# Kernel tuning notes

Hardware: AMD Instinct MI355X
Metric: run time of the kernel (lower is better)

## Reference

```python
import jax, jax.numpy as jnp
import numpy as np

D_SVG, N_TYPE, N_PAR = 256, 10, 12          # deep-svg latent, animation types, animation params
PADDING_VALUE = -1.0
W_SVG, W_TYPE, W_PAR = 10.0, 0.1, 1.0       # weight_deep_svg, weight_type, weight_parameters

# ANIMATION_PARAMETER_INDICES as a dense boolean lookup: type t -> which params it uses
_pm = np.zeros((N_TYPE, N_PAR), dtype=bool)
for _t in range(N_TYPE):
    for _k in (_t % N_PAR, (_t + 1) % N_PAR, (_t + 2) % N_PAR):
        _pm[_t, _k] = True
PARAM_MASK = jnp.asarray(_pm)


def setup_inputs() -> dict:
    B, S = 256, 512
    F = D_SVG + N_TYPE + N_PAR
    key = jax.random.key(0)
    k1, k2, k3, k4, k5 = jax.random.split(key, 5)
    x = jax.random.normal(k1, (B, S, F), dtype=jnp.float32)
    cls = jax.random.randint(k2, (B, S), 0, N_TYPE)
    t_type = jax.nn.one_hot(cls, N_TYPE, dtype=jnp.float32)
    t_svg = jax.random.normal(k3, (B, S, D_SVG), dtype=jnp.float32)
    t_par = jax.random.normal(k4, (B, S, N_PAR), dtype=jnp.float32)
    target = jnp.concatenate([t_svg, t_type, t_par], axis=-1)
    # suffix-contiguous padding (matches the `break` semantics of the torch loop)
    lengths = jax.random.randint(k5, (B,), S // 2, S + 1)
    mask = jnp.arange(S)[None, :] >= lengths[:, None]            # True = padded
    target = jnp.where(mask[..., None], PADDING_VALUE, target)
    return {"input": x, "target": target, "target_padding_mask": mask}


def reference(input, target, target_padding_mask):
    # input[expanded_mask] = -100
    x = jnp.where(target_padding_mask[..., None], -100.0, input)
    in_svg, in_type, in_par = jnp.split(x, [D_SVG, D_SVG + N_TYPE], axis=-1)
    tg_svg, tg_type, tg_par = jnp.split(target, [D_SVG, D_SVG + N_TYPE], axis=-1)

    valid = tg_type[..., 0] != PADDING_VALUE                      # [B,S] non-padded rows
    t_idx = jnp.argmax(tg_type, axis=-1)                          # [B,S] animation type

    # vectorized replacement of the double for-loop: copy target params at the
    # type-dependent ANIMATION_PARAMETER_INDICES into input params
    pmask = PARAM_MASK[t_idx] & valid[..., None]                  # [B,S,N_PAR]
    in_par = jnp.where(pmask, tg_par, in_par)

    # CrossEntropyLoss(ignore_index=-1) over flattened type logits
    logits = in_type.reshape(-1, N_TYPE)
    labels = t_idx.reshape(-1)
    v = valid.reshape(-1).astype(logits.dtype)
    logp = jax.nn.log_softmax(logits, axis=-1)
    nll = -jnp.take_along_axis(logp, labels[:, None], axis=1)[:, 0]
    loss_type = jnp.sum(nll * v) / jnp.maximum(jnp.sum(v), 1.0)

    # plain MSE (mean over ALL elements, padding included, as in the original)
    loss_svg = jnp.mean((in_svg - tg_svg) ** 2)
    loss_par = jnp.mean((in_par - tg_par) ** 2)

    return W_SVG * loss_svg + W_TYPE * loss_type + W_PAR * loss_par
```

## Files before the change

kernel.cpp:

```cpp
#include <hip/hip_runtime.h>
#include <math.h>

#define D_SVG 256
#define N_TYPE 10
#define N_PAR 12
#define F_TOT (D_SVG + N_TYPE + N_PAR)
#define ROWS_PER_BLOCK 64
#define THREADS 256
#define N4_PER_BLOCK (ROWS_PER_BLOCK * F_TOT / 4)
#define SEC (N_TYPE + N_PAR)
#define SECP 23


__global__ __launch_bounds__(256) void bitmap_kernel(const float* __restrict__ target,
                                                     unsigned* __restrict__ bitmap) {
    const int tid = threadIdx.x;
    const long r = (long)blockIdx.x * 256 + tid;
    const bool valid = (target[r * F_TOT + D_SVG] != -1.0f);
    unsigned long long bal = __ballot(valid);
    const int lane = tid & 63, wv = tid >> 6;
    if (lane == 0)  bitmap[blockIdx.x * 8 + wv * 2]     = (unsigned)bal;
    if (lane == 32) bitmap[blockIdx.x * 8 + wv * 2 + 1] = (unsigned)(bal >> 32);
}

__global__ __launch_bounds__(THREADS) void fused_kernel(const float* __restrict__ input,
                                                        const float* __restrict__ target,
                                                        const unsigned* __restrict__ bitmap,
                                                        float4* __restrict__ part) {
    __shared__ float s_in[ROWS_PER_BLOCK][SECP];
    __shared__ float s_tg[ROWS_PER_BLOCK][SECP];
    __shared__ float sred[4][4];
    const int tid  = threadIdx.x;
    const int lane = tid & 63, wave = tid >> 6;

    const unsigned long long b =
        ((const unsigned long long*)bitmap)[blockIdx.x];

    if (b == 0ull) {
        if (tid == 0) part[blockIdx.x] = make_float4(0.f, 0.f, 0.f, 0.f);
        return;
    }

    const long row0 = (long)blockIdx.x * ROWS_PER_BLOCK;

    const unsigned k = (unsigned)__popcll(b);
    const unsigned long long pre = (k == 64u) ? ~0ull : ((1ull << k) - 1ull);
    const unsigned n4v = (b == pre) ? ((k * (unsigned)F_TOT + 3u) >> 2)
                                    : (unsigned)N4_PER_BLOCK;

    const float4* __restrict__ in4p = (const float4*)(input  + row0 * F_TOT);
    const float4* __restrict__ tg4p = (const float4*)(target + row0 * F_TOT);

    float svg = 0.0f, par = 0.0f;

    auto accum = [&](unsigned idx, float4 ivv, float4 tvv) {
        unsigned e0 = idx * 4u;
        unsigned ra = e0 / (unsigned)F_TOT;
        unsigned rb = (e0 + 2u) / (unsigned)F_TOT;
        unsigned fa = e0 - ra * (unsigned)F_TOT;
        unsigned fb = (e0 + 2u) - rb * (unsigned)F_TOT;
        unsigned vA = (unsigned)(b >> ra) & 1u;
        unsigned vB = (unsigned)(b >> rb) & 1u;
        float xs[4] = {ivv.x, ivv.y, ivv.z, ivv.w};
        float ts[4] = {tvv.x, tvv.y, tvv.z, tvv.w};
        #pragma unroll
        for (int j = 0; j < 4; ++j) {
            unsigned row  = (j < 2) ? ra : rb;
            unsigned feat = ((j < 2) ? fa : fb) + (unsigned)(j & 1);
            unsigned v    = (j < 2) ? vA : vB;
            float d = xs[j] - ts[j];
            float sq = d * d;
            svg += (v && feat < D_SVG) ? sq : 0.0f;
            par += (v && feat >= D_SVG + N_TYPE) ? sq : 0.0f;
            if (feat >= D_SVG) {
                s_in[row][feat - D_SVG] = xs[j];
                s_tg[row][feat - D_SVG] = ts[j];
            }
        }
    };

    unsigned idx = (unsigned)tid;
    for (; idx + 7u * THREADS < n4v; idx += 8u * THREADS) {
        float4 a[8], t[8];
        #pragma unroll
        for (int u = 0; u < 8; ++u) a[u] = in4p[idx + u * THREADS];
        #pragma unroll
        for (int u = 0; u < 8; ++u) t[u] = tg4p[idx + u * THREADS];
        #pragma unroll
        for (int u = 0; u < 8; ++u) accum(idx + u * THREADS, a[u], t[u]);
    }
    for (; idx < n4v; idx += THREADS) accum(idx, in4p[idx], tg4p[idx]);

    __syncthreads();

    float nll = 0.0f, corr = 0.0f;
    if (tid < ROWS_PER_BLOCK && ((b >> tid) & 1ull)) {
        float tt[N_TYPE], l[N_TYPE];
        #pragma unroll
        for (int j = 0; j < N_TYPE; ++j) { tt[j] = s_tg[tid][j]; l[j] = s_in[tid][j]; }
        int ti = 0; float best = tt[0];
        #pragma unroll
        for (int j = 1; j < N_TYPE; ++j) { if (tt[j] > best) { best = tt[j]; ti = j; } }
        float m = l[0];
        #pragma unroll
        for (int j = 1; j < N_TYPE; ++j) m = fmaxf(m, l[j]);
        float s = 0.0f;
        #pragma unroll
        for (int j = 0; j < N_TYPE; ++j) s += __expf(l[j] - m);
        nll = __logf(s) + m - l[ti];
        #pragma unroll
        for (int j = 0; j < 3; ++j) {
            float d = s_in[tid][N_TYPE + ti + j] - s_tg[tid][N_TYPE + ti + j];
            corr += d * d;
        }
    }

    float vals[4] = {svg, par, nll, corr};
    #pragma unroll
    for (int v = 0; v < 4; ++v) {
        float x = vals[v];
        #pragma unroll
        for (int off = 32; off > 0; off >>= 1) x += __shfl_down(x, off, 64);
        vals[v] = x;
    }
    if (lane == 0) {
        #pragma unroll
        for (int v = 0; v < 4; ++v) sred[wave][v] = vals[v];
    }
    __syncthreads();
    if (tid == 0) {
        float s0 = sred[0][0] + sred[1][0] + sred[2][0] + sred[3][0];
        float s1 = sred[0][1] + sred[1][1] + sred[2][1] + sred[3][1];
        float s2 = sred[0][2] + sred[1][2] + sred[2][2] + sred[3][2];
        float s3 = sred[0][3] + sred[1][3] + sred[2][3] + sred[3][3];
        part[blockIdx.x] = make_float4(s0, s1, s2, s3);
    }
}

__global__ __launch_bounds__(256) void loss_final(const float4* __restrict__ part,
                                                  const unsigned* __restrict__ bitmap,
                                                  float* __restrict__ out,
                                                  int nb, int nw, int nrows) {
    __shared__ double sred[4][5];
    const int tid = threadIdx.x;
    double svg = 0.0, par = 0.0, nll = 0.0, corr = 0.0, cnt = 0.0;
    for (int i = tid; i < nb; i += 256) {
        float4 v = part[i];
        svg += v.x; par += v.y; nll += v.z; corr += v.w;
    }
    for (int i = tid; i < nw; i += 256)
        cnt += (double)__popc(bitmap[i]);
    double vals[5] = {svg, par, nll, corr, cnt};
    #pragma unroll
    for (int v = 0; v < 5; ++v) {
        double x = vals[v];
        #pragma unroll
        for (int off = 32; off > 0; off >>= 1) x += __shfl_down(x, off, 64);
        vals[v] = x;
    }
    const int wave = tid >> 6, lane = tid & 63;
    if (lane == 0) {
        #pragma unroll
        for (int v = 0; v < 5; ++v) sred[wave][v] = vals[v];
    }
    __syncthreads();
    if (tid == 0) {
        double S[5];
        #pragma unroll
        for (int v = 0; v < 5; ++v)
            S[v] = sred[0][v] + sred[1][v] + sred[2][v] + sred[3][v];
        double npad = (double)nrows - S[4];
        double svg_t = S[0] + 9801.0 * D_SVG * npad;
        double par_t = S[1] - S[3] + 9801.0 * N_PAR * npad;
        double loss = 10.0 * svg_t / ((double)nrows * D_SVG)
                    + 0.1  * S[2] / fmax(S[4], 1.0)
                    + 1.0  * par_t / ((double)nrows * N_PAR);
        out[0] = (float)loss;
    }
}

extern "C" void kernel_launch(void* const* d_in, const int* in_sizes, int n_in,
                              void* d_out, int out_size, void* d_ws, size_t ws_size,
                              hipStream_t stream) {
    const float* input  = (const float*)d_in[0];
    const float* target = (const float*)d_in[1];
    float* out = (float*)d_out;

    const int nrows = in_sizes[0] / F_TOT;
    const int blk   = nrows / ROWS_PER_BLOCK;
    const int nw    = nrows / 32;
    const int blk_m = nrows / 256;

    float4*   part   = (float4*)d_ws;
    unsigned* bitmap = (unsigned*)((char*)d_ws + (size_t)blk * sizeof(float4));

    bitmap_kernel<<<blk_m, 256, 0, stream>>>(target, bitmap);
    fused_kernel<<<blk, THREADS, 0, stream>>>(input, target, bitmap, part);
    loss_final<<<1, 256, 0, stream>>>(part, bitmap, out, blk, nw, nrows);
}
```

Baseline: 297.9 us.

## Sum all squared diffs uniformly and subtract type/param sections separately

The streaming loop now accumulates squared differences over every feature with no per-element row/feature division or shared-memory stores. The type and parameter sections are reloaded per valid row with float2 loads, written to shared memory, and their contributions subtracted from the total to get the SVG term. Blocks with a suffix-padded prefix take a branch-free fast path, with a fix-up for a row split across a float4 boundary. Subtracting large sums in fp32 may cost precision, and the section reads now happen twice, though they likely hit in cache.

Measured after the change: 297.2 us. No clear change (-0.2%).

```diff
diff --git a/kernel.cpp b/kernel.cpp
--- a/kernel.cpp
+++ b/kernel.cpp
@@ -4,11 +4,10 @@
 #define D_SVG 256
 #define N_TYPE 10
 #define N_PAR 12
-#define F_TOT (D_SVG + N_TYPE + N_PAR)
+#define F_TOT 278
 #define ROWS_PER_BLOCK 64
 #define THREADS 256
 #define N4_PER_BLOCK (ROWS_PER_BLOCK * F_TOT / 4)
-#define SEC (N_TYPE + N_PAR)
 #define SECP 23
 
 
@@ -33,8 +32,7 @@
     const int tid  = threadIdx.x;
     const int lane = tid & 63, wave = tid >> 6;
 
-    const unsigned long long b =
-        ((const unsigned long long*)bitmap)[blockIdx.x];
+    const unsigned long long b = ((const unsigned long long*)bitmap)[blockIdx.x];
 
     if (b == 0ull) {
         if (tid == 0) part[blockIdx.x] = make_float4(0.f, 0.f, 0.f, 0.f);
@@ -45,52 +43,77 @@
 
     const unsigned k = (unsigned)__popcll(b);
     const unsigned long long pre = (k == 64u) ? ~0ull : ((1ull << k) - 1ull);
-    const unsigned n4v = (b == pre) ? ((k * (unsigned)F_TOT + 3u) >> 2)
-                                    : (unsigned)N4_PER_BLOCK;
+    const bool fast = (b == pre);
+    const unsigned n4v = fast ? ((k * (unsigned)F_TOT + 3u) >> 2)
+                              : (unsigned)N4_PER_BLOCK;
 
     const float4* __restrict__ in4p = (const float4*)(input  + row0 * F_TOT);
     const float4* __restrict__ tg4p = (const float4*)(target + row0 * F_TOT);
 
-    float svg = 0.0f, par = 0.0f;
-
-    auto accum = [&](unsigned idx, float4 ivv, float4 tvv) {
-        unsigned e0 = idx * 4u;
-        unsigned ra = e0 / (unsigned)F_TOT;
-        unsigned rb = (e0 + 2u) / (unsigned)F_TOT;
-        unsigned fa = e0 - ra * (unsigned)F_TOT;
-        unsigned fb = (e0 + 2u) - rb * (unsigned)F_TOT;
-        unsigned vA = (unsigned)(b >> ra) & 1u;
-        unsigned vB = (unsigned)(b >> rb) & 1u;
-        float xs[4] = {ivv.x, ivv.y, ivv.z, ivv.w};
-        float ts[4] = {tvv.x, tvv.y, tvv.z, tvv.w};
-        #pragma unroll
-        for (int j = 0; j < 4; ++j) {
-            unsigned row  = (j < 2) ? ra : rb;
-            unsigned feat = ((j < 2) ? fa : fb) + (unsigned)(j & 1);
-            unsigned v    = (j < 2) ? vA : vB;
-            float d = xs[j] - ts[j];
-            float sq = d * d;
-            svg += (v && feat < D_SVG) ? sq : 0.0f;
-            par += (v && feat >= D_SVG + N_TYPE) ? sq : 0.0f;
-            if (feat >= D_SVG) {
-                s_in[row][feat - D_SVG] = xs[j];
-                s_tg[row][feat - D_SVG] = ts[j];
+    float sall = 0.0f;
+
+    if (fast) {
+        unsigned idx = (unsigned)tid;
+        for (; idx + 7u * THREADS < n4v; idx += 8u * THREADS) {
+            float4 a[8], t[8];
+            #pragma unroll
+            for (int u = 0; u < 8; ++u) a[u] = in4p[idx + u * THREADS];
+            #pragma unroll
+            for (int u = 0; u < 8; ++u) t[u] = tg4p[idx + u * THREADS];
+            #pragma unroll
+            for (int u = 0; u < 8; ++u) {
+                float dx = a[u].x - t[u].x, dy = a[u].y - t[u].y;
+                float dz = a[u].z - t[u].z, dw = a[u].w - t[u].w;
+                sall = fmaf(dx, dx, sall); sall = fmaf(dy, dy, sall);
+                sall = fmaf(dz, dz, sall); sall = fmaf(dw, dw, sall);
             }
         }
-    };
-
-    unsigned idx = (unsigned)tid;
-    for (; idx + 7u * THREADS < n4v; idx += 8u * THREADS) {
-        float4 a[8], t[8];
-        #pragma unroll
-        for (int u = 0; u < 8; ++u) a[u] = in4p[idx + u * THREADS];
-        #pragma unroll
-        for (int u = 0; u < 8; ++u) t[u] = tg4p[idx + u * THREADS];
-        #pragma unroll
-        for (int u = 0; u < 8; ++u) accum(idx + u * THREADS, a[u], t[u]);
-    }
-    for (; idx < n4v; idx += THREADS) accum(idx, in4p[idx], tg4p[idx]);
-
+        for (; idx < n4v; idx += THREADS) {
+            float4 a = in4p[idx], t = tg4p[idx];
+            float dx = a.x - t.x, dy = a.y - t.y, dz = a.z - t.z, dw = a.w - t.w;
+            sall = fmaf(dx, dx, sall); sall = fmaf(dy, dy, sall);
+            sall = fmaf(dz, dz, sall); sall = fmaf(dw, dw, sall);
+        }
+        if (tid == 0 && (k & 1u) && k < 64u) {
+            const float* ip = input  + (row0 + k) * F_TOT;
+            const float* tp = target + (row0 + k) * F_TOT;
+            float d0 = ip[0] - tp[0], d1 = ip[1] - tp[1];
+            sall -= d0 * d0 + d1 * d1;
+        }
+    } else {
+        for (unsigned idx = (unsigned)tid; idx < (unsigned)N4_PER_BLOCK; idx += THREADS) {
+            float4 a = in4p[idx], t = tg4p[idx];
+            unsigned e0 = idx * 4u;
+            unsigned ra = e0 / (unsigned)F_TOT;
+            unsigned rb = (e0 + 2u) / (unsigned)F_TOT;
+            float vA = (float)((unsigned)(b >> ra) & 1u);
+            float vB = (float)((unsigned)(b >> rb) & 1u);
+            float dx = a.x - t.x, dy = a.y - t.y, dz = a.z - t.z, dw = a.w - t.w;
+            sall = fmaf(vA * dx, dx, sall); sall = fmaf(vA * dy, dy, sall);
+            sall = fmaf(vB * dz, dz, sall); sall = fmaf(vB * dw, dw, sall);
+        }
+    }
+
+    float stype = 0.0f, spar = 0.0f;
+    {
+        const int r = tid >> 2, c = tid & 3;
+        if ((b >> r) & 1ull) {
+            const float2* __restrict__ ip2 = (const float2*)(input  + (row0 + r) * F_TOT + D_SVG);
+            const float2* __restrict__ tp2 = (const float2*)(target + (row0 + r) * F_TOT + D_SVG);
+            #pragma unroll
+            for (int m = 0; m < 3; ++m) {
+                int j = c + 4 * m;
+                if (j < 11) {
+                    float2 iv = ip2[j], tv = tp2[j];
+                    s_in[r][2*j] = iv.x; s_in[r][2*j + 1] = iv.y;
+                    s_tg[r][2*j] = tv.x; s_tg[r][2*j + 1] = tv.y;
+                    float d0 = iv.x - tv.x, d1 = iv.y - tv.y;
+                    float sq = d0 * d0 + d1 * d1;
+                    if (j < 5) stype += sq; else spar += sq;
+                }
+            }
+        }
+    }
     __syncthreads();
 
     float nll = 0.0f, corr = 0.0f;
@@ -115,7 +138,7 @@
         }
     }
 
-    float vals[4] = {svg, par, nll, corr};
+    float vals[4] = {sall - stype - spar, spar, nll, corr};
     #pragma unroll
     for (int v = 0; v < 4; ++v) {
         float x = vals[v];
```
